# Optimization experiments

Measured on AMD Instinct MI355X. Metric: run time of the kernel, lower is better.

## Reference

```python
import jax, jax.numpy as jnp
import numpy as np

OBS = 4096      # flattened observation size (hardcoded in down_sampler)
ENC = 1024      # encoding_size
LAT = 512       # policy_latent_size
ACT = 3         # action_space_n
B = 4096        # batch
NMAX = 8        # max neighbors (padded ragged dim)


def setup_inputs() -> dict:
    key = jax.random.key(0)
    ks = jax.random.split(key, 16)

    def w(i, shape, fan_in):
        return jax.random.normal(ks[i], shape, jnp.float32) * (1.0 / np.sqrt(fan_in))

    return {
        "observation": jax.random.normal(ks[0], (B, OBS), jnp.float32),
        "neighbors": jax.random.normal(ks[1], (B, NMAX, LAT), jnp.float32),
        "neighbor_counts": jax.random.randint(ks[2], (B,), 0, 9, jnp.int32),
        # down_sampler: Linear(4096, ENC) + ReLU
        "W_ds": w(3, (ENC, OBS), OBS), "b_ds": jnp.zeros((ENC,), jnp.float32),
        # policy: Linear(ENC, LAT) + ReLU
        "W_pol": w(4, (LAT, ENC), ENC), "b_pol": jnp.zeros((LAT,), jnp.float32),
        # v_net: Linear(ENC, 1) + Tanh
        "W_v": w(5, (1, ENC), ENC), "b_v": jnp.zeros((1,), jnp.float32),
        # GRUCell(LAT, LAT): weight_ih [3L, L], weight_hh [3L, L]
        "W_ih": w(6, (3 * LAT, LAT), LAT), "b_ih": jnp.zeros((3 * LAT,), jnp.float32),
        "W_hh": w(7, (3 * LAT, LAT), LAT), "b_hh": jnp.zeros((3 * LAT,), jnp.float32),
        # to_probs: Linear(LAT, ACT) + ReLU + Softmax
        "W_pr": w(8, (ACT, LAT), LAT), "b_pr": jnp.zeros((ACT,), jnp.float32),
    }


def _gru_cell(x, h, W_ih, b_ih, W_hh, b_hh):
    # PyTorch GRUCell semantics; gates ordered (r, z, n)
    gi = x @ W_ih.T + b_ih          # [B, 3L]
    gh = h @ W_hh.T + b_hh          # [B, 3L]
    i_r, i_z, i_n = jnp.split(gi, 3, axis=-1)
    h_r, h_z, h_n = jnp.split(gh, 3, axis=-1)
    r = jax.nn.sigmoid(i_r + h_r)
    z = jax.nn.sigmoid(i_z + h_z)
    n = jnp.tanh(i_n + r * h_n)
    return (1.0 - z) * n + z * h


def reference(observation, neighbors, neighbor_counts,
              W_ds, b_ds, W_pol, b_pol, W_v, b_v,
              W_ih, b_ih, W_hh, b_hh, W_pr, b_pr):
    # step 0: forward_initial
    enc = jax.nn.relu(observation @ W_ds.T + b_ds)        # [B, ENC]
    pol = jax.nn.relu(enc @ W_pol.T + b_pol)              # [B, LAT]
    state_vals = jnp.tanh(enc @ W_v.T + b_v)              # [B, 1]

    # step 1: forward_communicate -- ragged GRU recurrence over padded neighbors
    xs = jnp.swapaxes(neighbors, 0, 1)                    # [NMAX, B, LAT]
    ts = jnp.arange(NMAX)

    def step(h, xt):
        x, t = xt
        h_new = _gru_cell(x, h, W_ih, b_ih, W_hh, b_hh)
        valid = (t < neighbor_counts)[:, None]            # mask padded neighbor slots
        return jnp.where(valid, h_new, h), None

    h, _ = jax.lax.scan(step, pol, (xs, ts))              # [B, LAT]

    # step 2: forward_probs
    probs = jax.nn.softmax(jax.nn.relu(h @ W_pr.T + b_pr), axis=-1)  # [B, ACT]
    return probs, state_vals
```

## Files before the change

kernel.cpp:

```cpp
#include <hip/hip_runtime.h>
#include <hip/hip_bf16.h>

typedef __attribute__((ext_vector_type(8))) short short8;
typedef __attribute__((ext_vector_type(4))) float floatx4;

__device__ __forceinline__ ushort f2bf(float x) {
    unsigned u = __float_as_uint(x);
    unsigned r = (u + 0x7fffu + ((u >> 16) & 1u)) >> 16;
    return (ushort)r;
}
__device__ __forceinline__ float bf2f(ushort h) {
    return __uint_as_float(((unsigned)h) << 16);
}
__device__ __forceinline__ float fast_sigmoid(float x) {
    return 1.0f / (1.0f + __expf(-x));
}
__device__ __forceinline__ float fast_tanh(float x) {
    x = fminf(fmaxf(x, -15.0f), 15.0f);
    float e = __expf(2.0f * x);
    return (e - 1.0f) / (e + 1.0f);
}
__device__ __forceinline__ void load_lds16(const void* g, void* l) {
    __builtin_amdgcn_global_load_lds(
        (__attribute__((address_space(1))) void*)(g),
        (__attribute__((address_space(3))) void*)(l),
        16, 0, 0);
}

__device__ __forceinline__ void stage_unit(const ushort* grow0, int ld, ushort* lds_unit) {
    const int lane = threadIdx.x & 63;
    const int r = lane >> 3;
    const int c = (lane & 7) ^ r;
    load_lds16(grow0 + (size_t)r * ld + c * 8, lds_unit);
}
__device__ __forceinline__ short8 lds_read8(const ushort* buf, int R, int c_el) {
    const int idx = ((R >> 3) << 9) + ((R & 7) << 6) + ((((c_el >> 3) ^ (R & 7))) << 3);
    return *(const short8*)(buf + idx);
}

__global__ __launch_bounds__(256) void cvt_all(
    const float* __restrict__ s0, ushort* __restrict__ d0,
    const float* __restrict__ s1, ushort* __restrict__ d1,
    const float* __restrict__ s2, ushort* __restrict__ d2,
    const float* __restrict__ s3, ushort* __restrict__ d3,
    const float* __restrict__ s4, ushort* __restrict__ d4) {
    int i = blockIdx.x * 256 + threadIdx.x;
    const float* s;
    ushort* d;
    int j;
    if (i < 4194304)      { s = s0; d = d0; j = i; }
    else if (i < 5242880) { s = s1; d = d1; j = i - 4194304; }
    else if (i < 5373952) { s = s2; d = d2; j = i - 5242880; }
    else if (i < 5570560) { s = s3; d = d3; j = i - 5373952; }
    else if (i < 5767168) { s = s4; d = d4; j = i - 5570560; }
    else return;
    const float4 v = ((const float4*)s)[j];
    ushort4 o;
    o.x = f2bf(v.x); o.y = f2bf(v.y); o.z = f2bf(v.z); o.w = f2bf(v.w);
    ((ushort4*)d)[j] = o;
}

__global__ __launch_bounds__(256) void cvt_f32_bf16(const float* __restrict__ src,
                                                    ushort* __restrict__ dst, int n4) {
    int i = blockIdx.x * blockDim.x + threadIdx.x;
    if (i >= n4) return;
    const float4 v = ((const float4*)src)[i];
    ushort4 o;
    o.x = f2bf(v.x); o.y = f2bf(v.y); o.z = f2bf(v.z); o.w = f2bf(v.w);
    ((ushort4*)dst)[i] = o;
}

__global__ __launch_bounds__(256) void sort_by_cnt(const int* __restrict__ cnt,
                                                   int* __restrict__ perm,
                                                   int* __restrict__ inv,
                                                   int* __restrict__ nact) {
    __shared__ int h[9];
    __shared__ int cur[9];
    const int tid = threadIdx.x;
    if (tid < 9) h[tid] = 0;
    __syncthreads();
    for (int i = tid; i < 4096; i += 256) atomicAdd(&h[cnt[i]], 1);
    __syncthreads();
    if (tid == 0) {
        int off = 0;
        for (int c = 8; c >= 0; --c) { cur[c] = off; off += h[c]; }
        for (int t = 0; t < 8; ++t) {
            int n = 0;
            for (int c = t + 1; c <= 8; ++c) n += h[c];
            nact[t] = n;
        }
    }
    __syncthreads();
    for (int i = tid; i < 4096; i += 256) {
        const int c = cnt[i];
        const int p = atomicAdd(&cur[c], 1);
        perm[p] = i;
        inv[i] = p;
    }
}

template <int MODE, int BN, int KSPLIT, bool MAP>
__global__ __launch_bounds__(256, 2) void gemm64(
    const ushort* __restrict__ A, int lda,
    const ushort* __restrict__ B, int ldb,
    const float* __restrict__ bias,
    const int* __restrict__ row_map,
    ushort* __restrict__ Cb, float* __restrict__ Cf, int ldc,
    int K, size_t part_stride) {
    __shared__ __attribute__((aligned(16))) ushort sA[64 * 64];
    __shared__ __attribute__((aligned(16))) ushort sB[BN * 64];

    constexpr int NJ = (BN + 63) / 64;
    constexpr int UB = BN / 32;

    const int tid = threadIdx.x;
    const int lane = tid & 63;
    const int w = tid >> 6;
    const int m0 = blockIdx.y * 64;
    const int n0 = blockIdx.x * BN;
    const int wn = w * (16 * NJ);
    const int nl = lane & 15;

    const int Kper = K / KSPLIT;
    const int kbase = (KSPLIT > 1) ? blockIdx.z * Kper : 0;
    if (MODE == 3) Cf += (size_t)blockIdx.z * part_stride;

    floatx4 acc[4][NJ] = {};

    for (int k0 = kbase; k0 < kbase + Kper; k0 += 64) {
#pragma unroll
        for (int u = 0; u < 2; ++u) {
            const int ua = w * 2 + u;
            stage_unit(A + (size_t)(m0 + ua * 8) * lda + k0, lda, &sA[ua * 512]);
        }
#pragma unroll
        for (int u = 0; u < UB; ++u) {
            const int ub = w * UB + u;
            stage_unit(B + (size_t)(n0 + ub * 8) * ldb + k0, ldb, &sB[ub * 512]);
        }
        __syncthreads();
#pragma unroll
        for (int kk = 0; kk < 2; ++kk) {
            const int cb = kk * 32 + (lane >> 4) * 8;
            short8 a[4], b[NJ];
#pragma unroll
            for (int i = 0; i < 4; ++i) a[i] = lds_read8(sA, i * 16 + nl, cb);
#pragma unroll
            for (int j = 0; j < NJ; ++j) b[j] = lds_read8(sB, wn + j * 16 + nl, cb);
#pragma unroll
            for (int i = 0; i < 4; ++i)
#pragma unroll
                for (int j = 0; j < NJ; ++j)
                    acc[i][j] = __builtin_amdgcn_mfma_f32_16x16x32_bf16(a[i], b[j], acc[i][j], 0, 0, 0);
        }
        __syncthreads();
    }

    const int ml = (lane >> 4) * 4;
#pragma unroll
    for (int j = 0; j < NJ; ++j) {
        const int n = n0 + wn + j * 16 + nl;
        float bv = 0.0f;
        if (MODE == 2) bv = bias[n];
#pragma unroll
        for (int i = 0; i < 4; ++i) {
            const int mbase = m0 + i * 16 + ml;
#pragma unroll
            for (int r = 0; r < 4; ++r) {
                float v = acc[i][j][r];
                const int mr = mbase + r;
                const int orow = MAP ? row_map[mr] : mr;
                const size_t off = (size_t)orow * ldc + n;
                if (MODE == 2) {
                    v += bv; v = fmaxf(v, 0.0f);
                    Cb[off] = f2bf(v);
                    Cf[off] = v;
                } else {
                    Cf[off] = v;
                }
            }
        }
    }
}

__global__ __launch_bounds__(256) void combine_relu(const float* __restrict__ p0,
                                                    const float* __restrict__ p1,
                                                    const float* __restrict__ bias,
                                                    ushort* __restrict__ ob, int n4) {
    int i = blockIdx.x * blockDim.x + threadIdx.x;
    if (i >= n4) return;
    const float4 a = ((const float4*)p0)[i];
    const float4 b = ((const float4*)p1)[i];
    const int col = (i * 4) & 1023;
    const float4 bs = *(const float4*)(bias + col);
    ushort4 o;
    o.x = f2bf(fmaxf(a.x + b.x + bs.x, 0.f));
    o.y = f2bf(fmaxf(a.y + b.y + bs.y, 0.f));
    o.z = f2bf(fmaxf(a.z + b.z + bs.z, 0.f));
    o.w = f2bf(fmaxf(a.w + b.w + bs.w, 0.f));
    ((ushort4*)ob)[i] = o;
}

__global__ __launch_bounds__(512, 2) void gru_step(
    const ushort* __restrict__ Xall,
    const ushort* __restrict__ Hin,
    const ushort* __restrict__ Wih,
    const ushort* __restrict__ Whh,
    const float* __restrict__ bih, const float* __restrict__ bhh,
    const int* __restrict__ perm, const int* __restrict__ nact,
    float* __restrict__ hf, ushort* __restrict__ Hout, int t) {
    extern __shared__ __attribute__((aligned(16))) ushort smem[];
    ushort* sX   = smem;
    ushort* sH   = sX + 8192;
    ushort* sBih = sH + 8192;
    ushort* sBhh = sBih + 12288;

    const int tid = threadIdx.x;
    const int lane = tid & 63;
    const int w = tid >> 6;
    const int wr = w >> 2;
    const int wc = w & 3;
    const int s = blockIdx.x;
    const int m0 = blockIdx.y * 128;
    const int na = nact[t];
    if (m0 >= na) return;

    const int nl = lane & 15;
    const int ml = (lane >> 4) * 4;
    const int col = s * 64 + wc * 16 + nl;

    const int r = lane >> 3;
    const int c = (lane & 7) ^ r;
    const ushort* xb[2];
    const ushort* hbp[2];
#pragma unroll
    for (int u = 0; u < 2; ++u) {
        const int ua = w * 2 + u;
        const int srow = m0 + ua * 8 + r;
        const int orig = perm[srow];
        xb[u] = Xall + (size_t)orig * 4096 + t * 512 + c * 8;
        hbp[u] = Hin + (size_t)srow * 512 + c * 8;
    }
    const ushort* wi[3];
    const ushort* wh[3];
#pragma unroll
    for (int j = 0; j < 3; ++j) {
        const int uw = w * 3 + j;
        const int grow = (uw >> 3) * 512 + s * 64 + (uw & 7) * 8 + r;
        wi[j] = Wih + (size_t)grow * 512 + c * 8;
        wh[j] = Whh + (size_t)grow * 512 + c * 8;
    }

    floatx4 accr[4], accz[4], accn[4], acch[4];
    {
        const float br_ = bih[col] + bhh[col];
        const float bz_ = bih[512 + col] + bhh[512 + col];
        const float bn_i = bih[1024 + col];
        const float bn_h = bhh[1024 + col];
        const floatx4 vr = {br_, br_, br_, br_};
        const floatx4 vz = {bz_, bz_, bz_, bz_};
        const floatx4 vi = {bn_i, bn_i, bn_i, bn_i};
        const floatx4 vh = {bn_h, bn_h, bn_h, bn_h};
#pragma unroll
        for (int i = 0; i < 4; ++i) { accr[i] = vr; accz[i] = vz; accn[i] = vi; acch[i] = vh; }
    }

    for (int k0 = 0; k0 < 512; k0 += 64) {
#pragma unroll
        for (int u = 0; u < 2; ++u) {
            const int ua = w * 2 + u;
            load_lds16(xb[u] + k0, &sX[ua * 512]);
            load_lds16(hbp[u] + k0, &sH[ua * 512]);
        }
#pragma unroll
        for (int j = 0; j < 3; ++j) {
            const int uw = w * 3 + j;
            load_lds16(wi[j] + k0, &sBih[uw * 512]);
            load_lds16(wh[j] + k0, &sBhh[uw * 512]);
        }
        __syncthreads();
#pragma unroll
        for (int kk = 0; kk < 2; ++kk) {
            const int cb = kk * 32 + (lane >> 4) * 8;
            short8 ax[4], ah[4];
#pragma unroll
            for (int i = 0; i < 4; ++i) {
                ax[i] = lds_read8(sX, wr * 64 + i * 16 + nl, cb);
                ah[i] = lds_read8(sH, wr * 64 + i * 16 + nl, cb);
            }
            const short8 bir = lds_read8(sBih, wc * 16 + nl, cb);
            const short8 biz = lds_read8(sBih, 64 + wc * 16 + nl, cb);
            const short8 bin = lds_read8(sBih, 128 + wc * 16 + nl, cb);
            const short8 bhr = lds_read8(sBhh, wc * 16 + nl, cb);
            const short8 bhz = lds_read8(sBhh, 64 + wc * 16 + nl, cb);
            const short8 bhn = lds_read8(sBhh, 128 + wc * 16 + nl, cb);
#pragma unroll
            for (int i = 0; i < 4; ++i) {
                accr[i] = __builtin_amdgcn_mfma_f32_16x16x32_bf16(ax[i], bir, accr[i], 0, 0, 0);
                accr[i] = __builtin_amdgcn_mfma_f32_16x16x32_bf16(ah[i], bhr, accr[i], 0, 0, 0);
                accz[i] = __builtin_amdgcn_mfma_f32_16x16x32_bf16(ax[i], biz, accz[i], 0, 0, 0);
                accz[i] = __builtin_amdgcn_mfma_f32_16x16x32_bf16(ah[i], bhz, accz[i], 0, 0, 0);
                accn[i] = __builtin_amdgcn_mfma_f32_16x16x32_bf16(ax[i], bin, accn[i], 0, 0, 0);
                acch[i] = __builtin_amdgcn_mfma_f32_16x16x32_bf16(ah[i], bhn, acch[i], 0, 0, 0);
            }
        }
        __syncthreads();
    }

    const bool full = (m0 + 128 <= na);
    const int rbase = m0 + wr * 64;
#pragma unroll
    for (int i = 0; i < 4; ++i) {
#pragma unroll
        for (int r4 = 0; r4 < 4; ++r4) {
            const int row = rbase + i * 16 + ml + r4;
            const float rg = fast_sigmoid(accr[i][r4]);
            const float zg = fast_sigmoid(accz[i][r4]);
            const float ng = fast_tanh(accn[i][r4] + rg * acch[i][r4]);
            const size_t off = (size_t)row * 512 + col;
            const float ho = hf[off];
            const bool act = full || (row < na);
            const float hv = act ? ((1.0f - zg) * ng + zg * ho) : ho;
            hf[off] = hv;
            if (t < 7) Hout[off] = f2bf(hv);
        }
    }
}

__global__ __launch_bounds__(256) void v_kernel(const ushort* __restrict__ enc,
                                                const float* __restrict__ Wv,
                                                const float* __restrict__ bv,
                                                float* __restrict__ out) {
    const int row = blockIdx.x * 4 + (threadIdx.x >> 6);
    const int lane = threadIdx.x & 63;
    const ushort* e = enc + (size_t)row * 1024;
    float s = 0.0f;
#pragma unroll
    for (int i = 0; i < 16; ++i) {
        int k = lane + i * 64;
        s += bf2f(e[k]) * Wv[k];
    }
#pragma unroll
    for (int off = 32; off; off >>= 1) s += __shfl_down(s, off, 64);
    if (lane == 0) out[row] = fast_tanh(s + bv[0]);
}

__global__ __launch_bounds__(256) void probs_kernel(const float* __restrict__ h,
                                                    const float* __restrict__ Wpr,
                                                    const float* __restrict__ bpr,
                                                    const int* __restrict__ perm,
                                                    float* __restrict__ out) {
    const int srow = blockIdx.x * 4 + (threadIdx.x >> 6);
    const int lane = threadIdx.x & 63;
    const float* hr = h + (size_t)srow * 512;
    float p0 = 0.f, p1 = 0.f, p2 = 0.f;
#pragma unroll
    for (int i = 0; i < 8; ++i) {
        int k = lane + i * 64;
        float x = hr[k];
        p0 += x * Wpr[k];
        p1 += x * Wpr[512 + k];
        p2 += x * Wpr[1024 + k];
    }
#pragma unroll
    for (int off = 32; off; off >>= 1) {
        p0 += __shfl_down(p0, off, 64);
        p1 += __shfl_down(p1, off, 64);
        p2 += __shfl_down(p2, off, 64);
    }
    if (lane == 0) {
        const int orow = perm[srow];
        p0 = fmaxf(p0 + bpr[0], 0.f);
        p1 = fmaxf(p1 + bpr[1], 0.f);
        p2 = fmaxf(p2 + bpr[2], 0.f);
        float m = fmaxf(p0, fmaxf(p1, p2));
        float e0 = __expf(p0 - m), e1 = __expf(p1 - m), e2 = __expf(p2 - m);
        float inv = 1.0f / (e0 + e1 + e2);
        out[orow * 3 + 0] = e0 * inv;
        out[orow * 3 + 1] = e1 * inv;
        out[orow * 3 + 2] = e2 * inv;
    }
}

extern "C" void kernel_launch(void* const* d_in, const int* in_sizes, int n_in,
                              void* d_out, int out_size, void* d_ws, size_t ws_size,
                              hipStream_t stream) {
    const float* obs   = (const float*)d_in[0];
    const float* nbr   = (const float*)d_in[1];
    const int*   cnt   = (const int*)d_in[2];
    const float* W_ds  = (const float*)d_in[3];
    const float* b_ds  = (const float*)d_in[4];
    const float* W_pol = (const float*)d_in[5];
    const float* b_pol = (const float*)d_in[6];
    const float* W_v   = (const float*)d_in[7];
    const float* b_v   = (const float*)d_in[8];
    const float* W_ih  = (const float*)d_in[9];
    const float* b_ih  = (const float*)d_in[10];
    const float* W_hh  = (const float*)d_in[11];
    const float* b_hh  = (const float*)d_in[12];
    const float* W_pr  = (const float*)d_in[13];
    const float* b_pr  = (const float*)d_in[14];
    float* out = (float*)d_out;

    ushort* obs_b  = (ushort*)d_ws;
    ushort* Wds_b  = obs_b + 16777216;
    ushort* Wpol_b = Wds_b + 4194304;
    ushort* Wih_b  = Wpol_b + 524288;
    ushort* Whh_b  = Wih_b + 786432;
    ushort* enc_b  = Whh_b + 786432;
    ushort* h_b0   = enc_b + 4194304;
    ushort* h_b1   = h_b0 + 2097152;
    float*  h_f    = (float*)(h_b1 + 2097152);
    float*  part   = h_f + 2097152;
    ushort* nbr_b  = (ushort*)part;
    int*    perm   = (int*)(part + 8388608);
    int*    inv    = perm + 4096;
    int*    nact   = inv + 4096;

    static bool attr_done = false;
    if (!attr_done) {
        hipFuncSetAttribute((const void*)gru_step,
                            hipFuncAttributeMaxDynamicSharedMemorySize, 81920);
        attr_done = true;
    }

    sort_by_cnt<<<1, 256, 0, stream>>>(cnt, perm, inv, nact);

    cvt_all<<<22528, 256, 0, stream>>>(obs, obs_b, W_ds, Wds_b, W_pol, Wpol_b,
                                       W_ih, Wih_b, W_hh, Whh_b);

    gemm64<3, 128, 2, false><<<dim3(8, 64, 2), 256, 0, stream>>>(
        obs_b, 4096, Wds_b, 4096, nullptr, nullptr, nullptr, part, 1024, 4096, 4194304);
    combine_relu<<<4096, 256, 0, stream>>>(part, part + 4194304, b_ds, enc_b, 1048576);

    cvt_f32_bf16<<<16384, 256, 0, stream>>>(nbr, nbr_b, 4194304);

    gemm64<2, 64, 1, true><<<dim3(8, 64, 1), 256, 0, stream>>>(
        enc_b, 1024, Wpol_b, 1024, b_pol, inv, h_b0, h_f, 512, 1024, 0);

    v_kernel<<<1024, 256, 0, stream>>>(enc_b, W_v, b_v, out + 12288);

    for (int t = 0; t < 8; ++t) {
        const ushort* hin = (t & 1) ? h_b1 : h_b0;
        ushort* hout = (t & 1) ? h_b0 : h_b1;
        gru_step<<<dim3(8, 32), 512, 81920, stream>>>(nbr_b, hin, Wih_b, Whh_b,
                                                      b_ih, b_hh, perm, nact, h_f, hout, t);
    }

    probs_kernel<<<1024, 256, 0, stream>>>(h_f, W_pr, b_pr, perm, out);
}
```

Measured before the change: 474.4 us.

## Replace LDS-staged GRU step with direct global-to-register MFMA operand loads

The GRU step kernel drops its shared-memory staging and barriers. Each wave now loads its bf16 A and B MFMA fragments straight from global memory into registers, using smaller 64-row tiles, 256-thread blocks and twice as many blocks. This removes LDS traffic and synchronisation and lets more blocks run at once. In exchange, weights and activations are no longer shared through LDS across waves, so there is more redundant global/L2 traffic with small strided 16-byte loads.

```diff
diff --git a/kernel.cpp b/kernel.cpp
--- a/kernel.cpp
+++ b/kernel.cpp
@@ -201,7 +201,7 @@
     ((ushort4*)ob)[i] = o;
 }
 
-__global__ __launch_bounds__(512, 2) void gru_step(
+__global__ __launch_bounds__(256) void gru_step(
     const ushort* __restrict__ Xall,
     const ushort* __restrict__ Hin,
     const ushort* __restrict__ Wih,
@@ -209,47 +209,33 @@
     const float* __restrict__ bih, const float* __restrict__ bhh,
     const int* __restrict__ perm, const int* __restrict__ nact,
     float* __restrict__ hf, ushort* __restrict__ Hout, int t) {
-    extern __shared__ __attribute__((aligned(16))) ushort smem[];
-    ushort* sX   = smem;
-    ushort* sH   = sX + 8192;
-    ushort* sBih = sH + 8192;
-    ushort* sBhh = sBih + 12288;
-
     const int tid = threadIdx.x;
     const int lane = tid & 63;
     const int w = tid >> 6;
-    const int wr = w >> 2;
-    const int wc = w & 3;
     const int s = blockIdx.x;
-    const int m0 = blockIdx.y * 128;
+    const int m0 = blockIdx.y * 64;
     const int na = nact[t];
     if (m0 >= na) return;
 
     const int nl = lane & 15;
+    const int kq = (lane >> 4) * 8;
     const int ml = (lane >> 4) * 4;
-    const int col = s * 64 + wc * 16 + nl;
-
-    const int r = lane >> 3;
-    const int c = (lane & 7) ^ r;
-    const ushort* xb[2];
-    const ushort* hbp[2];
-#pragma unroll
-    for (int u = 0; u < 2; ++u) {
-        const int ua = w * 2 + u;
-        const int srow = m0 + ua * 8 + r;
-        const int orig = perm[srow];
-        xb[u] = Xall + (size_t)orig * 4096 + t * 512 + c * 8;
-        hbp[u] = Hin + (size_t)srow * 512 + c * 8;
-    }
-    const ushort* wi[3];
-    const ushort* wh[3];
-#pragma unroll
-    for (int j = 0; j < 3; ++j) {
-        const int uw = w * 3 + j;
-        const int grow = (uw >> 3) * 512 + s * 64 + (uw & 7) * 8 + r;
-        wi[j] = Wih + (size_t)grow * 512 + c * 8;
-        wh[j] = Whh + (size_t)grow * 512 + c * 8;
-    }
+    const int col = s * 64 + w * 16 + nl;
+
+    const ushort* xa[4];
+    const ushort* ha[4];
+#pragma unroll
+    for (int i = 0; i < 4; ++i) {
+        const int srow = m0 + i * 16 + nl;
+        xa[i] = Xall + (size_t)perm[srow] * 4096 + t * 512 + kq;
+        ha[i] = Hin + (size_t)srow * 512 + kq;
+    }
+    const ushort* bi0 = Wih + (size_t)col * 512 + kq;
+    const ushort* bi1 = Wih + (size_t)(512 + col) * 512 + kq;
+    const ushort* bi2 = Wih + (size_t)(1024 + col) * 512 + kq;
+    const ushort* bh0 = Whh + (size_t)col * 512 + kq;
+    const ushort* bh1 = Whh + (size_t)(512 + col) * 512 + kq;
+    const ushort* bh2 = Whh + (size_t)(1024 + col) * 512 + kq;
 
     floatx4 accr[4], accz[4], accn[4], acch[4];
     {
@@ -265,55 +251,38 @@
         for (int i = 0; i < 4; ++i) { accr[i] = vr; accz[i] = vz; accn[i] = vi; acch[i] = vh; }
     }
 
-    for (int k0 = 0; k0 < 512; k0 += 64) {
-#pragma unroll
-        for (int u = 0; u < 2; ++u) {
-            const int ua = w * 2 + u;
-            load_lds16(xb[u] + k0, &sX[ua * 512]);
-            load_lds16(hbp[u] + k0, &sH[ua * 512]);
-        }
-#pragma unroll
-        for (int j = 0; j < 3; ++j) {
-            const int uw = w * 3 + j;
-            load_lds16(wi[j] + k0, &sBih[uw * 512]);
-            load_lds16(wh[j] + k0, &sBhh[uw * 512]);
-        }
-        __syncthreads();
-#pragma unroll
-        for (int kk = 0; kk < 2; ++kk) {
-            const int cb = kk * 32 + (lane >> 4) * 8;
-            short8 ax[4], ah[4];
-#pragma unroll
-            for (int i = 0; i < 4; ++i) {
-                ax[i] = lds_read8(sX, wr * 64 + i * 16 + nl, cb);
-                ah[i] = lds_read8(sH, wr * 64 + i * 16 + nl, cb);
-            }
-            const short8 bir = lds_read8(sBih, wc * 16 + nl, cb);
-            const short8 biz = lds_read8(sBih, 64 + wc * 16 + nl, cb);
-            const short8 bin = lds_read8(sBih, 128 + wc * 16 + nl, cb);
-            const short8 bhr = lds_read8(sBhh, wc * 16 + nl, cb);
-            const short8 bhz = lds_read8(sBhh, 64 + wc * 16 + nl, cb);
-            const short8 bhn = lds_read8(sBhh, 128 + wc * 16 + nl, cb);
-#pragma unroll
-            for (int i = 0; i < 4; ++i) {
-                accr[i] = __builtin_amdgcn_mfma_f32_16x16x32_bf16(ax[i], bir, accr[i], 0, 0, 0);
-                accr[i] = __builtin_amdgcn_mfma_f32_16x16x32_bf16(ah[i], bhr, accr[i], 0, 0, 0);
-                accz[i] = __builtin_amdgcn_mfma_f32_16x16x32_bf16(ax[i], biz, accz[i], 0, 0, 0);
-                accz[i] = __builtin_amdgcn_mfma_f32_16x16x32_bf16(ah[i], bhz, accz[i], 0, 0, 0);
-                accn[i] = __builtin_amdgcn_mfma_f32_16x16x32_bf16(ax[i], bin, accn[i], 0, 0, 0);
-                acch[i] = __builtin_amdgcn_mfma_f32_16x16x32_bf16(ah[i], bhn, acch[i], 0, 0, 0);
-            }
-        }
-        __syncthreads();
-    }
-
-    const bool full = (m0 + 128 <= na);
-    const int rbase = m0 + wr * 64;
+#pragma unroll
+    for (int c = 0; c < 16; ++c) {
+        const int ko = c * 32;
+        short8 ax[4], ah[4];
+#pragma unroll
+        for (int i = 0; i < 4; ++i) {
+            ax[i] = *(const short8*)(xa[i] + ko);
+            ah[i] = *(const short8*)(ha[i] + ko);
+        }
+        const short8 bir = *(const short8*)(bi0 + ko);
+        const short8 biz = *(const short8*)(bi1 + ko);
+        const short8 bin = *(const short8*)(bi2 + ko);
+        const short8 bhr = *(const short8*)(bh0 + ko);
+        const short8 bhz = *(const short8*)(bh1 + ko);
+        const short8 bhn = *(const short8*)(bh2 + ko);
+#pragma unroll
+        for (int i = 0; i < 4; ++i) {
+            accr[i] = __builtin_amdgcn_mfma_f32_16x16x32_bf16(ax[i], bir, accr[i], 0, 0, 0);
+            accr[i] = __builtin_amdgcn_mfma_f32_16x16x32_bf16(ah[i], bhr, accr[i], 0, 0, 0);
+            accz[i] = __builtin_amdgcn_mfma_f32_16x16x32_bf16(ax[i], biz, accz[i], 0, 0, 0);
+            accz[i] = __builtin_amdgcn_mfma_f32_16x16x32_bf16(ah[i], bhz, accz[i], 0, 0, 0);
+            accn[i] = __builtin_amdgcn_mfma_f32_16x16x32_bf16(ax[i], bin, accn[i], 0, 0, 0);
+            acch[i] = __builtin_amdgcn_mfma_f32_16x16x32_bf16(ah[i], bhn, acch[i], 0, 0, 0);
+        }
+    }
+
+    const bool full = (m0 + 64 <= na);
 #pragma unroll
     for (int i = 0; i < 4; ++i) {
 #pragma unroll
         for (int r4 = 0; r4 < 4; ++r4) {
-            const int row = rbase + i * 16 + ml + r4;
+            const int row = m0 + i * 16 + ml + r4;
             const float rg = fast_sigmoid(accr[i][r4]);
             const float zg = fast_sigmoid(accz[i][r4]);
             const float ng = fast_tanh(accn[i][r4] + rg * acch[i][r4]);
@@ -417,13 +386,6 @@
     int*    inv    = perm + 4096;
     int*    nact   = inv + 4096;
 
-    static bool attr_done = false;
-    if (!attr_done) {
-        hipFuncSetAttribute((const void*)gru_step,
-                            hipFuncAttributeMaxDynamicSharedMemorySize, 81920);
-        attr_done = true;
-    }
-
     sort_by_cnt<<<1, 256, 0, stream>>>(cnt, perm, inv, nact);
 
     cvt_all<<<22528, 256, 0, stream>>>(obs, obs_b, W_ds, Wds_b, W_pol, Wpol_b,
@@ -443,8 +405,8 @@
     for (int t = 0; t < 8; ++t) {
         const ushort* hin = (t & 1) ? h_b1 : h_b0;
         ushort* hout = (t & 1) ? h_b0 : h_b1;
-        gru_step<<<dim3(8, 32), 512, 81920, stream>>>(nbr_b, hin, Wih_b, Whh_b,
-                                                      b_ih, b_hh, perm, nact, h_f, hout, t);
+        gru_step<<<dim3(8, 64), 256, 0, stream>>>(nbr_b, hin, Wih_b, Whh_b,
+                                                  b_ih, b_hh, perm, nact, h_f, hout, t);
     }
 
     probs_kernel<<<1024, 256, 0, stream>>>(h_f, W_pr, b_pr, perm, out);
```

After: 635.6 us. 1.34x slower.
